# Performance work log

Measured on AMD Instinct MI355X. Metric: run time of the kernel, lower is better.

## Reference

```python
import jax, jax.numpy as jnp
import numpy as np

N, F_IN, HID, HEADS, NEA, E, G = 50000, 32, 64, 2, 2, 800000, 50
SLOPE = 0.2  # leaky_relu negative_slope


def setup_inputs() -> dict:
    key = jax.random.key(0)
    ks = jax.random.split(key, 24)
    x = jax.random.normal(ks[0], (N, F_IN), jnp.float32)
    src = jax.random.randint(ks[1], (E,), 0, N, jnp.int32)
    off = jax.random.randint(ks[2], (E,), 1, N, jnp.int32)
    dst = ((src + off) % N).astype(jnp.int32)  # guaranteed no self loops
    edge_index = jnp.stack([src, dst])
    edge_attr = jax.random.uniform(ks[3], (E, NEA), jnp.float32, 0.5, 3.0)  # distances (reciprocal taken in fwd)
    batch = (jnp.arange(N) // (N // G)).astype(jnp.int32)
    interface_pos = jnp.arange(0, N, 5, dtype=jnp.int32)  # 200 interface nodes/graph

    def glorot(k, shape, fan_in, fan_out):
        s = jnp.sqrt(6.0 / (fan_in + fan_out))
        return jax.random.uniform(k, shape, jnp.float32, -s, s)

    HC = HEADS * HID
    W0 = glorot(ks[4], (F_IN, HC), F_IN, HC)
    attl0 = glorot(ks[5], (HEADS, HID), HID, HID)
    attr0 = glorot(ks[6], (HEADS, HID), HID, HID)
    W12 = glorot(ks[7], (2, HID, HC), HID, HC)
    attl12 = glorot(ks[8], (2, HEADS, HID), HID, HID)
    attr12 = glorot(ks[9], (2, HEADS, HID), HID, HID)
    eW = glorot(ks[10], (3, NEA, HC), NEA, HC)
    eb = jnp.zeros((3, HC), jnp.float32)
    bconv = jnp.zeros((3, HID), jnp.float32)
    gate_w = glorot(ks[11], (HID, 1), HID, 1)
    gate_b = jnp.zeros((1,), jnp.float32)
    lin1_w = glorot(ks[12], (4 * HID, 2 * HID), 4 * HID, 2 * HID)
    lin1_b = jnp.zeros((2 * HID,), jnp.float32)
    lin2_w = glorot(ks[13], (2 * HID, 1), 2 * HID, 1)
    lin2_b = jnp.zeros((1,), jnp.float32)
    return dict(x=x, edge_index=edge_index, edge_attr=edge_attr, batch=batch,
                interface_pos=interface_pos, graph_num=G,
                W0=W0, attl0=attl0, attr0=attr0, W12=W12, attl12=attl12, attr12=attr12,
                eW=eW, eb=eb, bconv=bconv, gate_w=gate_w, gate_b=gate_b,
                lin1_w=lin1_w, lin1_b=lin1_b, lin2_w=lin2_w, lin2_b=lin2_b)


def segment_softmax(e, seg, n):
    m = jax.ops.segment_max(e, seg, num_segments=n)
    ex = jnp.exp(e - m[seg])
    d = jax.ops.segment_sum(ex, seg, num_segments=n)
    return ex / (d[seg] + 1e-16)


def gate_conv(h, W, att_l, att_r, eW, eb, b, src, dst, ea):
    # GATEConv, concat=False, dropout in eval mode (identity)
    n = h.shape[0]
    H, C = att_l.shape
    xl = (h @ W).reshape(n, H, C)                      # lin_l == lin_r
    al = (xl * att_l).sum(-1)                          # [N,H]
    ar = (xl * att_r).sum(-1)
    e = jax.nn.leaky_relu(al[src] + ar[dst], SLOPE)    # [E+N,H]
    alpha = segment_softmax(e, dst, n)
    ee = (ea @ eW + eb).reshape(-1, H, C)              # edge embeddings
    msg = (xl[src] + ee) * alpha[..., None]
    out = jax.ops.segment_sum(msg, dst, num_segments=n)
    return out.mean(1) + b                             # mean over heads + bias


def reference(x, edge_index, edge_attr, batch, interface_pos, graph_num,
              W0, attl0, attr0, W12, attl12, attr12, eW, eb, bconv,
              gate_w, gate_b, lin1_w, lin1_b, lin2_w, lin2_b):
    n = x.shape[0]
    ar_n = jnp.arange(n, dtype=edge_index.dtype)
    src = jnp.concatenate([edge_index[0], ar_n])       # add self loops
    dst = jnp.concatenate([edge_index[1], ar_n])
    ea = jnp.concatenate([1.0 / edge_attr,
                          jnp.zeros((n, edge_attr.shape[1]), edge_attr.dtype)], 0)

    h = jnp.tanh(gate_conv(x, W0, attl0, attr0, eW[0], eb[0], bconv[0], src, dst, ea))
    xmax = h
    for l in range(2):  # num_layers - 1 structurally distinct weight slices
        h = jnp.tanh(gate_conv(h, W12[l], attl12[l], attr12[l],
                               eW[l + 1], eb[l + 1], bconv[l + 1], src, dst, ea))
        xmax = jnp.maximum(xmax, h)                    # JumpingKnowledge('max')

    xi = xmax[interface_pos]                           # [Ni, hidden]
    bi = batch[interface_pos]
    add = jax.ops.segment_sum(xi, bi, num_segments=graph_num)
    cnt = jax.ops.segment_sum(jnp.ones((xi.shape[0],), xi.dtype), bi, num_segments=graph_num)
    mean = add / jnp.maximum(cnt, 1.0)[:, None]
    gate = (xi @ gate_w + gate_b)[:, 0]                # global self-attention gate
    a = segment_softmax(gate, bi, graph_num)
    attp = jax.ops.segment_sum(a[:, None] * xi, bi, num_segments=graph_num)
    mx = jax.ops.segment_max(xi, bi, num_segments=graph_num)
    pooled = jnp.concatenate([add, mean, attp, mx], -1)  # [G, 4*hidden]
    z = jnp.tanh(pooled @ lin1_w + lin1_b)             # dropout eval = identity
    return z @ lin2_w + lin2_b                         # [G, 1]
```

## Files before the change

kernel.cpp:

```cpp
#include <hip/hip_runtime.h>
#include <hip/hip_bf16.h>
#include <hip/hip_fp16.h>
#include <math.h>

#define N_NODES 50000
#define FIN     32
#define HID     64
#define HC      128
#define NE      800000
#define NET     850000
#define NI      10000
#define NG      50
#define PB      8

__device__ __forceinline__ float lrelu(float x) { return x > 0.f ? x : 0.2f * x; }

__device__ __forceinline__ unsigned fenc(float f) {
  unsigned u = __float_as_uint(f);
  return (u & 0x80000000u) ? ~u : (u | 0x80000000u);
}
__device__ __forceinline__ float fdec(unsigned u) {
  return (u & 0x80000000u) ? __uint_as_float(u ^ 0x80000000u) : __uint_as_float(~u);
}

__device__ __forceinline__ float rlf(float v, int l) {
  return __int_as_float(__builtin_amdgcn_readlane(__float_as_int(v), l));
}
__device__ __forceinline__ int rli(int v, int l) {
  return __builtin_amdgcn_readlane(v, l);
}

__global__ void k_histrank(const int* __restrict__ ei, int* __restrict__ deg,
                           int* __restrict__ rank) {
  int e = blockIdx.x * blockDim.x + threadIdx.x;
  if (e >= NET) return;
  int d = (e < NE) ? ei[NE + e] : (e - NE);
  rank[e] = atomicAdd(&deg[d], 1);
}

__global__ void k_base(const int* __restrict__ deg, int* __restrict__ start,
                       int* __restrict__ gcur) {
  __shared__ int buf[256];
  __shared__ int basesh;
  int t = threadIdx.x;
  int i = blockIdx.x * 256 + t;
  int v = (i < N_NODES) ? deg[i] : 0;
  buf[t] = v; __syncthreads();
  for (int off = 1; off < 256; off <<= 1) {
    int a = (t >= off) ? buf[t - off] : 0;
    __syncthreads();
    buf[t] += a;
    __syncthreads();
  }
  if (t == 255) basesh = atomicAdd(gcur, buf[255]);
  __syncthreads();
  if (i < N_NODES) start[i] = basesh + buf[t] - v;
}

__global__ void k_scatter(const int* __restrict__ ei, const float* __restrict__ eattr,
                          const int* __restrict__ start, const int* __restrict__ rank,
                          int2* __restrict__ erec) {
  int e = blockIdx.x * blockDim.x + threadIdx.x;
  if (e >= NET) return;
  int s, d; float ex, ey;
  if (e < NE) {
    s = ei[e]; d = ei[NE + e];
    float2 ea = ((const float2*)eattr)[e];
    ex = 1.0f / ea.x; ey = 1.0f / ea.y;
  } else {
    s = d = e - NE; ex = 0.f; ey = 0.f;
  }
  int pos = start[d] + rank[e];
  __half2 ea2 = __floats2half2_rn(ex, ey);
  erec[pos] = make_int2(s, *(int*)&ea2);
}

template <int F>
__global__ void k_linear(const float* __restrict__ h, const float* __restrict__ W,
                         const float* __restrict__ attl, const float* __restrict__ attr,
                         __half2* __restrict__ xl2h, float* __restrict__ al,
                         float* __restrict__ ar) {
  __shared__ float lds[4][HC];
  const int c = threadIdx.x;
  const int head = c >> 6;
  const int cc = c & 63;
  float wcol[F];
#pragma unroll
  for (int k = 0; k < F; k++) wcol[k] = W[k * HC + c];
  const float attlv = attl[c];
  const float attrv = attr[c];
  for (int g = blockIdx.x; g < N_NODES / 4; g += gridDim.x) {
    const int n0 = g * 4;
    float acc[4] = {0.f, 0.f, 0.f, 0.f};
#pragma unroll
    for (int k4 = 0; k4 < F / 4; k4++) {
      float4 h4[4];
#pragma unroll
      for (int j = 0; j < 4; j++)
        h4[j] = *(const float4*)&h[(n0 + j) * F + k4 * 4];
#pragma unroll
      for (int j = 0; j < 4; j++) {
        acc[j] += h4[j].x * wcol[k4 * 4 + 0];
        acc[j] += h4[j].y * wcol[k4 * 4 + 1];
        acc[j] += h4[j].z * wcol[k4 * 4 + 2];
        acc[j] += h4[j].w * wcol[k4 * 4 + 3];
      }
    }
#pragma unroll
    for (int j = 0; j < 4; j++) {
      float lv = acc[j] * attlv, rv = acc[j] * attrv;
#pragma unroll
      for (int off = 32; off; off >>= 1) {
        lv += __shfl_xor(lv, off, 64);
        rv += __shfl_xor(rv, off, 64);
      }
      if (cc == 0) {
        al[(n0 + j) * 2 + head] = lv;
        ar[(n0 + j) * 2 + head] = rv;
      }
    }
    __syncthreads();
#pragma unroll
    for (int j = 0; j < 4; j++) lds[j][c] = acc[j];
    __syncthreads();
#pragma unroll
    for (int r = 0; r < 2; r++) {
      int idx = c + r * 128;
      int j = idx >> 6, ccc = idx & 63;
      xl2h[(size_t)(n0 + j) * HID + ccc] =
          __floats2half2_rn(lds[j][ccc], lds[j][64 + ccc]);
    }
  }
}

__global__ void k_aggregate(const __half2* __restrict__ xl2h, const float2* __restrict__ al2,
                            const float2* __restrict__ ar2, const int* __restrict__ start,
                            const int* __restrict__ degarr, const int2* __restrict__ erec,
                            const float* __restrict__ eW2, const float* __restrict__ eb1,
                            const float* __restrict__ bconv1, float* __restrict__ hout) {
  const int gid = blockIdx.x * 4 + (threadIdx.x >> 6);
  if (gid >= N_NODES) return;
  const int lane = threadIdx.x & 63;
  const int o0 = start[gid];
  const int deg = degarr[gid];
  const float2 arv = ar2[gid];

  float accA0 = 0.f, accA1 = 0.f, accB0 = 0.f, accB1 = 0.f;
  float ld0 = 0.f, ld1 = 0.f, lex0 = 0.f, ley0 = 0.f, lex1 = 0.f, ley1 = 0.f;
  for (int base = 0; base < deg; base += 64) {
    int j = base + lane;
    int s = 0; float p0 = 0.f, p1 = 0.f;
    if (j < deg) {
      int2 r = erec[o0 + j];
      s = r.x;
      float2 eaf = __half22float2(*(__half2*)&r.y);
      float2 alv = al2[s];
      p0 = __expf(lrelu(alv.x + arv.x));
      p1 = __expf(lrelu(alv.y + arv.y));
      ld0 += p0; ld1 += p1;
      lex0 += p0 * eaf.x; ley0 += p0 * eaf.y;
      lex1 += p1 * eaf.x; ley1 += p1 * eaf.y;
    }
    int slen = min(64, deg - base);
    int j2 = 0;
    for (; j2 + 8 <= slen; j2 += 8) {
      float2 x0 = __half22float2(xl2h[(size_t)rli(s, j2)     * HID + lane]);
      float2 x1 = __half22float2(xl2h[(size_t)rli(s, j2 + 1) * HID + lane]);
      float2 x2 = __half22float2(xl2h[(size_t)rli(s, j2 + 2) * HID + lane]);
      float2 x3 = __half22float2(xl2h[(size_t)rli(s, j2 + 3) * HID + lane]);
      float2 x4 = __half22float2(xl2h[(size_t)rli(s, j2 + 4) * HID + lane]);
      float2 x5 = __half22float2(xl2h[(size_t)rli(s, j2 + 5) * HID + lane]);
      float2 x6 = __half22float2(xl2h[(size_t)rli(s, j2 + 6) * HID + lane]);
      float2 x7 = __half22float2(xl2h[(size_t)rli(s, j2 + 7) * HID + lane]);
      accA0 += rlf(p0, j2)     * x0.x; accA1 += rlf(p1, j2)     * x0.y;
      accB0 += rlf(p0, j2 + 1) * x1.x; accB1 += rlf(p1, j2 + 1) * x1.y;
      accA0 += rlf(p0, j2 + 2) * x2.x; accA1 += rlf(p1, j2 + 2) * x2.y;
      accB0 += rlf(p0, j2 + 3) * x3.x; accB1 += rlf(p1, j2 + 3) * x3.y;
      accA0 += rlf(p0, j2 + 4) * x4.x; accA1 += rlf(p1, j2 + 4) * x4.y;
      accB0 += rlf(p0, j2 + 5) * x5.x; accB1 += rlf(p1, j2 + 5) * x5.y;
      accA0 += rlf(p0, j2 + 6) * x6.x; accA1 += rlf(p1, j2 + 6) * x6.y;
      accB0 += rlf(p0, j2 + 7) * x7.x; accB1 += rlf(p1, j2 + 7) * x7.y;
    }
    for (; j2 + 4 <= slen; j2 += 4) {
      float2 x0 = __half22float2(xl2h[(size_t)rli(s, j2)     * HID + lane]);
      float2 x1 = __half22float2(xl2h[(size_t)rli(s, j2 + 1) * HID + lane]);
      float2 x2 = __half22float2(xl2h[(size_t)rli(s, j2 + 2) * HID + lane]);
      float2 x3 = __half22float2(xl2h[(size_t)rli(s, j2 + 3) * HID + lane]);
      accA0 += rlf(p0, j2)     * x0.x; accA1 += rlf(p1, j2)     * x0.y;
      accB0 += rlf(p0, j2 + 1) * x1.x; accB1 += rlf(p1, j2 + 1) * x1.y;
      accA0 += rlf(p0, j2 + 2) * x2.x; accA1 += rlf(p1, j2 + 2) * x2.y;
      accB0 += rlf(p0, j2 + 3) * x3.x; accB1 += rlf(p1, j2 + 3) * x3.y;
    }
    for (; j2 < slen; j2++) {
      float2 x0 = __half22float2(xl2h[(size_t)rli(s, j2) * HID + lane]);
      accA0 += rlf(p0, j2) * x0.x; accA1 += rlf(p1, j2) * x0.y;
    }
  }
  float acc0 = accA0 + accB0, acc1 = accA1 + accB1;
#pragma unroll
  for (int off = 32; off; off >>= 1) {
    ld0  += __shfl_xor(ld0, off, 64);
    ld1  += __shfl_xor(ld1, off, 64);
    lex0 += __shfl_xor(lex0, off, 64);
    ley0 += __shfl_xor(ley0, off, 64);
    lex1 += __shfl_xor(lex1, off, 64);
    ley1 += __shfl_xor(ley1, off, 64);
  }
  float t0 = acc0 + eW2[lane]      * lex0 + eW2[HC + lane]      * ley0 + eb1[lane]      * ld0;
  float t1 = acc1 + eW2[64 + lane] * lex1 + eW2[HC + 64 + lane] * ley1 + eb1[64 + lane] * ld1;
  float r = 0.5f * (t0 / (ld0 + 1e-16f) + t1 / (ld1 + 1e-16f)) + bconv1[lane];
  hout[(size_t)gid * HID + lane] = tanhf(r);
}

__global__ void k_ranges(const int* __restrict__ ipos, const int* __restrict__ batch,
                         int* __restrict__ gstart) {
  int i = blockIdx.x * blockDim.x + threadIdx.x;
  if (i >= NI) return;
  int bi = batch[ipos[i]];
  int prev = (i > 0) ? batch[ipos[i - 1]] : -1;
  for (int g = prev + 1; g <= bi; g++) gstart[g] = i;
  if (i == NI - 1)
    for (int g = bi + 1; g <= NG; g++) gstart[g] = NI;
}

__global__ void k_pool(const float* __restrict__ h0, const float* __restrict__ h1,
                       const float* __restrict__ h2, const int* __restrict__ ipos,
                       const int* __restrict__ gstart, const float* __restrict__ gate_w,
                       const float* __restrict__ gate_b, float* __restrict__ add,
                       unsigned* __restrict__ mxE, float* __restrict__ cnt,
                       float* __restrict__ attp, float* __restrict__ aden) {
  __shared__ float red[4][3 * HID + 2];
  const int g = blockIdx.x / PB, m = blockIdx.x % PB;
  const int w = threadIdx.x >> 6, lane = threadIdx.x & 63;
  const int s0 = gstart[g], s1 = gstart[g + 1];
  const int len = s1 - s0;
  const int b0 = s0 + (len * m) / PB;
  const int b1 = s0 + (len * (m + 1)) / PB;
  const float gwv = gate_w[lane];
  const float gbv = gate_b[0];

  float padd = 0.f, pmax = -1e30f, pattp = 0.f, paden = 0.f, pcnt = 0.f;
  for (int i = b0 + w; i < b1; i += 4) {
    size_t node = (size_t)ipos[i] * HID + lane;
    float v = fmaxf(fmaxf(h0[node], h1[node]), h2[node]);
    padd += v;
    pmax = fmaxf(pmax, v);
    float gv = v * gwv;
#pragma unroll
    for (int off = 32; off; off >>= 1) gv += __shfl_xor(gv, off, 64);
    float e = __expf(gv + gbv);
    pattp += e * v;
    paden += e;
    pcnt += 1.f;
  }
  red[w][lane] = padd;
  red[w][HID + lane] = pmax;
  red[w][2 * HID + lane] = pattp;
  if (lane == 0) { red[w][3 * HID] = paden; red[w][3 * HID + 1] = pcnt; }
  __syncthreads();
  if (w == 0) {
    float addv  = red[0][lane] + red[1][lane] + red[2][lane] + red[3][lane];
    float maxv  = fmaxf(fmaxf(red[0][HID + lane], red[1][HID + lane]),
                        fmaxf(red[2][HID + lane], red[3][HID + lane]));
    float attpv = red[0][2 * HID + lane] + red[1][2 * HID + lane] +
                  red[2][2 * HID + lane] + red[3][2 * HID + lane];
    atomicAdd(&add[g * HID + lane], addv);
    atomicMax(&mxE[g * HID + lane], fenc(maxv));
    atomicAdd(&attp[g * HID + lane], attpv);
    if (lane == 0) {
      atomicAdd(&aden[g], red[0][3 * HID] + red[1][3 * HID] + red[2][3 * HID] + red[3][3 * HID]);
      atomicAdd(&cnt[g],  red[0][3 * HID + 1] + red[1][3 * HID + 1] +
                          red[2][3 * HID + 1] + red[3][3 * HID + 1]);
    }
  }
}

__global__ void k_final(const float* __restrict__ add, const float* __restrict__ cnt,
                        const float* __restrict__ attp, const float* __restrict__ aden,
                        const unsigned* __restrict__ mxE, const float* __restrict__ lin1_w,
                        const float* __restrict__ lin1_b, const float* __restrict__ lin2_w,
                        const float* __restrict__ lin2_b, float* __restrict__ out) {
  __shared__ float pooled[4 * HID];
  __shared__ float zred[2 * HID];
  int g = blockIdx.x, t = threadIdx.x;
  if (t < HID)            pooled[t] = add[g * HID + t];
  else if (t < 2 * HID)   pooled[t] = add[g * HID + (t - HID)] / fmaxf(cnt[g], 1.f);
  else if (t < 3 * HID)   pooled[t] = attp[g * HID + (t - 2 * HID)] / (aden[g] + 1e-16f);
  else                    pooled[t] = fdec(mxE[g * HID + (t - 3 * HID)]);
  __syncthreads();
  if (t < 2 * HID) {
    float z = lin1_b[t];
    for (int k = 0; k < 4 * HID; k++) z += pooled[k] * lin1_w[k * (2 * HID) + t];
    z = tanhf(z);
    zred[t] = z * lin2_w[t];
  }
  __syncthreads();
  if (t == 0) {
    float s = 0.f;
    for (int k = 0; k < 2 * HID; k++) s += zred[k];
    out[g] = s + lin2_b[0];
  }
}

extern "C" void kernel_launch(void* const* d_in, const int* in_sizes, int n_in,
                              void* d_out, int out_size, void* d_ws, size_t ws_size,
                              hipStream_t stream) {
  const float* x      = (const float*)d_in[0];
  const int*   ei     = (const int*)d_in[1];
  const float* eattr  = (const float*)d_in[2];
  const int*   batch  = (const int*)d_in[3];
  const int*   ipos   = (const int*)d_in[4];
  const float* W0     = (const float*)d_in[6];
  const float* attl0  = (const float*)d_in[7];
  const float* attr0  = (const float*)d_in[8];
  const float* W12    = (const float*)d_in[9];
  const float* attl12 = (const float*)d_in[10];
  const float* attr12 = (const float*)d_in[11];
  const float* eW     = (const float*)d_in[12];
  const float* eb     = (const float*)d_in[13];
  const float* bconv  = (const float*)d_in[14];
  const float* gate_w = (const float*)d_in[15];
  const float* gate_b = (const float*)d_in[16];
  const float* lin1_w = (const float*)d_in[17];
  const float* lin1_b = (const float*)d_in[18];
  const float* lin2_w = (const float*)d_in[19];
  const float* lin2_b = (const float*)d_in[20];
  float* out = (float*)d_out;

  char* ws = (char*)d_ws;
  size_t off = 0;
  auto alloc = [&](size_t elems) {
    void* p = ws + off;
    off += ((elems * 4 + 15) / 16) * 16;
    return p;
  };
  int*      deg    = (int*)alloc(N_NODES);
  int*      gcur   = (int*)alloc(4);
  float*    addp   = (float*)alloc(NG * HID);
  float*    attp   = (float*)alloc(NG * HID);
  unsigned* mxE    = (unsigned*)alloc(NG * HID);
  float*    cnt    = (float*)alloc(64);
  float*    aden   = (float*)alloc(64);
  size_t zbytes = off;
  int*     gstart = (int*)alloc(NG + 4);
  int*     start  = (int*)alloc(N_NODES);
  int*     rank   = (int*)alloc(NET);
  int2*    erec   = (int2*)alloc((size_t)NET * 2);
  __half2* xl2h   = (__half2*)alloc((size_t)N_NODES * HID);
  float*   al     = (float*)alloc((size_t)N_NODES * 2);
  float*   arr    = (float*)alloc((size_t)N_NODES * 2);
  float*   h0     = (float*)alloc((size_t)N_NODES * HID);
  float*   h1     = (float*)alloc((size_t)N_NODES * HID);
  float*   h2     = (float*)alloc((size_t)N_NODES * HID);
  (void)ws_size; (void)in_sizes; (void)n_in; (void)out_size;

  hipMemsetAsync(d_ws, 0, zbytes, stream);
  k_histrank<<<(NET + 255) / 256, 256, 0, stream>>>(ei, deg, rank);
  k_base<<<(N_NODES + 255) / 256, 256, 0, stream>>>(deg, start, gcur);
  k_scatter<<<(NET + 255) / 256, 256, 0, stream>>>(ei, eattr, start, rank, erec);
  k_ranges<<<(NI + 255) / 256, 256, 0, stream>>>(ipos, batch, gstart);

  k_linear<FIN><<<2500, 128, 0, stream>>>(x, W0, attl0, attr0, xl2h, al, arr);
  k_aggregate<<<N_NODES / 4, 256, 0, stream>>>(xl2h, (const float2*)al, (const float2*)arr,
                                               start, deg, erec, eW, eb, bconv, h0);
  k_linear<HID><<<2500, 128, 0, stream>>>(h0, W12, attl12, attr12, xl2h, al, arr);
  k_aggregate<<<N_NODES / 4, 256, 0, stream>>>(xl2h, (const float2*)al, (const float2*)arr,
                                               start, deg, erec, eW + 2 * HC, eb + HC,
                                               bconv + HID, h1);
  k_linear<HID><<<2500, 128, 0, stream>>>(h1, W12 + (size_t)HID * HC,
                                          attl12 + HC, attr12 + HC, xl2h, al, arr);
  k_aggregate<<<N_NODES / 4, 256, 0, stream>>>(xl2h, (const float2*)al, (const float2*)arr,
                                               start, deg, erec, eW + 4 * HC, eb + 2 * HC,
                                               bconv + 2 * HID, h2);

  k_pool<<<NG * PB, 256, 0, stream>>>(h0, h1, h2, ipos, gstart, gate_w, gate_b,
                                      addp, mxE, cnt, attp, aden);
  k_final<<<NG, 256, 0, stream>>>(addp, cnt, attp, aden, mxE, lin1_w, lin1_b, lin2_w, lin2_b, out);
}
```

Baseline: 393.5 us.

## Use MFMA fp16 for node linear and pre-scaled byte offsets in aggregation

New measurement: 341.6 us. -13.2%, faster.

```diff
diff --git a/kernel.cpp b/kernel.cpp
--- a/kernel.cpp
+++ b/kernel.cpp
@@ -13,7 +13,10 @@
 #define NG      50
 #define PB      8
 
-__device__ __forceinline__ float lrelu(float x) { return x > 0.f ? x : 0.2f * x; }
+typedef _Float16 half8 __attribute__((ext_vector_type(8)));
+typedef float float4v __attribute__((ext_vector_type(4)));
+
+__device__ __forceinline__ float lrelu(float x) { return fmaxf(x, 0.2f * x); }
 
 __device__ __forceinline__ unsigned fenc(float f) {
   unsigned u = __float_as_uint(f);
@@ -72,68 +75,88 @@
   }
   int pos = start[d] + rank[e];
   __half2 ea2 = __floats2half2_rn(ex, ey);
-  erec[pos] = make_int2(s, *(int*)&ea2);
+  erec[pos] = make_int2(s << 8, *(int*)&ea2);
 }
 
 template <int F>
-__global__ void k_linear(const float* __restrict__ h, const float* __restrict__ W,
-                         const float* __restrict__ attl, const float* __restrict__ attr,
-                         __half2* __restrict__ xl2h, float* __restrict__ al,
-                         float* __restrict__ ar) {
-  __shared__ float lds[4][HC];
-  const int c = threadIdx.x;
-  const int head = c >> 6;
-  const int cc = c & 63;
-  float wcol[F];
-#pragma unroll
-  for (int k = 0; k < F; k++) wcol[k] = W[k * HC + c];
-  const float attlv = attl[c];
-  const float attrv = attr[c];
-  for (int g = blockIdx.x; g < N_NODES / 4; g += gridDim.x) {
-    const int n0 = g * 4;
-    float acc[4] = {0.f, 0.f, 0.f, 0.f};
-#pragma unroll
-    for (int k4 = 0; k4 < F / 4; k4++) {
-      float4 h4[4];
-#pragma unroll
-      for (int j = 0; j < 4; j++)
-        h4[j] = *(const float4*)&h[(n0 + j) * F + k4 * 4];
-#pragma unroll
-      for (int j = 0; j < 4; j++) {
-        acc[j] += h4[j].x * wcol[k4 * 4 + 0];
-        acc[j] += h4[j].y * wcol[k4 * 4 + 1];
-        acc[j] += h4[j].z * wcol[k4 * 4 + 2];
-        acc[j] += h4[j].w * wcol[k4 * 4 + 3];
-      }
-    }
-#pragma unroll
-    for (int j = 0; j < 4; j++) {
-      float lv = acc[j] * attlv, rv = acc[j] * attrv;
-#pragma unroll
-      for (int off = 32; off; off >>= 1) {
-        lv += __shfl_xor(lv, off, 64);
-        rv += __shfl_xor(rv, off, 64);
-      }
-      if (cc == 0) {
-        al[(n0 + j) * 2 + head] = lv;
-        ar[(n0 + j) * 2 + head] = rv;
-      }
-    }
-    __syncthreads();
-#pragma unroll
-    for (int j = 0; j < 4; j++) lds[j][c] = acc[j];
-    __syncthreads();
-#pragma unroll
-    for (int r = 0; r < 2; r++) {
-      int idx = c + r * 128;
-      int j = idx >> 6, ccc = idx & 63;
-      xl2h[(size_t)(n0 + j) * HID + ccc] =
-          __floats2half2_rn(lds[j][ccc], lds[j][64 + ccc]);
-    }
-  }
-}
-
-__global__ void k_aggregate(const __half2* __restrict__ xl2h, const float2* __restrict__ al2,
+__global__ __launch_bounds__(256) void k_linear_mfma(
+    const float* __restrict__ h, const float* __restrict__ W,
+    const float* __restrict__ attl, const float* __restrict__ attr,
+    __half2* __restrict__ xl2h, float* __restrict__ al, float* __restrict__ ar) {
+  __shared__ _Float16 hA[16 * F];
+  __shared__ _Float16 hC[16 * 128];
+  __shared__ float redl[16 * 4], redr[16 * 4];
+  const int w = threadIdx.x >> 6, lane = threadIdx.x & 63;
+  const int m = lane & 15, q = lane >> 4;
+  const int n0 = blockIdx.x * 16;
+
+  for (int i = threadIdx.x; i < 16 * F; i += 256)
+    hA[i] = (_Float16)h[(size_t)n0 * F + i];
+  __syncthreads();
+
+  half8 a0, a1;
+#pragma unroll
+  for (int j = 0; j < 8; j++) a0[j] = hA[m * F + q * 8 + j];
+  if constexpr (F == 64) {
+#pragma unroll
+    for (int j = 0; j < 8; j++) a1[j] = hA[m * F + 32 + q * 8 + j];
+  }
+
+  const int c0 = w * 32;
+  float4v acc[2];
+  float pl[4] = {0.f, 0.f, 0.f, 0.f}, pr[4] = {0.f, 0.f, 0.f, 0.f};
+#pragma unroll
+  for (int t = 0; t < 2; t++) {
+    const int colg = c0 + t * 16 + m;
+    half8 b0;
+#pragma unroll
+    for (int j = 0; j < 8; j++) b0[j] = (_Float16)W[(q * 8 + j) * HC + colg];
+    float4v z = {0.f, 0.f, 0.f, 0.f};
+    acc[t] = __builtin_amdgcn_mfma_f32_16x16x32_f16(a0, b0, z, 0, 0, 0);
+    if constexpr (F == 64) {
+      half8 b1;
+#pragma unroll
+      for (int j = 0; j < 8; j++) b1[j] = (_Float16)W[(32 + q * 8 + j) * HC + colg];
+      acc[t] = __builtin_amdgcn_mfma_f32_16x16x32_f16(a1, b1, acc[t], 0, 0, 0);
+    }
+    const float atl = attl[colg], atr = attr[colg];
+#pragma unroll
+    for (int reg = 0; reg < 4; reg++) {
+      float val = acc[t][reg];
+      hC[(q * 4 + reg) * 128 + colg] = (_Float16)val;
+      pl[reg] += val * atl;
+      pr[reg] += val * atr;
+    }
+  }
+#pragma unroll
+  for (int off = 1; off < 16; off <<= 1) {
+#pragma unroll
+    for (int reg = 0; reg < 4; reg++) {
+      pl[reg] += __shfl_xor(pl[reg], off, 64);
+      pr[reg] += __shfl_xor(pr[reg], off, 64);
+    }
+  }
+  if (m == 0) {
+#pragma unroll
+    for (int reg = 0; reg < 4; reg++) {
+      redl[(q * 4 + reg) * 4 + w] = pl[reg];
+      redr[(q * 4 + reg) * 4 + w] = pr[reg];
+    }
+  }
+  __syncthreads();
+  if (threadIdx.x < 32) {
+    int node = threadIdx.x >> 1, head = threadIdx.x & 1;
+    al[(n0 + node) * 2 + head] = redl[node * 4 + head * 2] + redl[node * 4 + head * 2 + 1];
+    ar[(n0 + node) * 2 + head] = redr[node * 4 + head * 2] + redr[node * 4 + head * 2 + 1];
+  }
+  for (int i = threadIdx.x; i < 16 * 64; i += 256) {
+    int node = i >> 6, cc = i & 63;
+    xl2h[(size_t)(n0 + node) * HID + cc] =
+        __halves2half2(hC[node * 128 + cc], hC[node * 128 + 64 + cc]);
+  }
+}
+
+__global__ void k_aggregate(const __half2* __restrict__ xl2h, const float* __restrict__ alp,
                             const float2* __restrict__ ar2, const int* __restrict__ start,
                             const int* __restrict__ degarr, const int2* __restrict__ erec,
                             const float* __restrict__ eW2, const float* __restrict__ eb1,
@@ -141,20 +164,23 @@
   const int gid = blockIdx.x * 4 + (threadIdx.x >> 6);
   if (gid >= N_NODES) return;
   const int lane = threadIdx.x & 63;
+  const int lane4 = lane << 2;
   const int o0 = start[gid];
   const int deg = degarr[gid];
   const float2 arv = ar2[gid];
+  const char* xbase = (const char*)xl2h;
+  const char* albase = (const char*)alp;
 
   float accA0 = 0.f, accA1 = 0.f, accB0 = 0.f, accB1 = 0.f;
   float ld0 = 0.f, ld1 = 0.f, lex0 = 0.f, ley0 = 0.f, lex1 = 0.f, ley1 = 0.f;
   for (int base = 0; base < deg; base += 64) {
     int j = base + lane;
-    int s = 0; float p0 = 0.f, p1 = 0.f;
+    int soff = 0; float p0 = 0.f, p1 = 0.f;
     if (j < deg) {
       int2 r = erec[o0 + j];
-      s = r.x;
+      soff = r.x;
       float2 eaf = __half22float2(*(__half2*)&r.y);
-      float2 alv = al2[s];
+      float2 alv = *(const float2*)(albase + (soff >> 5));
       p0 = __expf(lrelu(alv.x + arv.x));
       p1 = __expf(lrelu(alv.y + arv.y));
       ld0 += p0; ld1 += p1;
@@ -164,14 +190,14 @@
     int slen = min(64, deg - base);
     int j2 = 0;
     for (; j2 + 8 <= slen; j2 += 8) {
-      float2 x0 = __half22float2(xl2h[(size_t)rli(s, j2)     * HID + lane]);
-      float2 x1 = __half22float2(xl2h[(size_t)rli(s, j2 + 1) * HID + lane]);
-      float2 x2 = __half22float2(xl2h[(size_t)rli(s, j2 + 2) * HID + lane]);
-      float2 x3 = __half22float2(xl2h[(size_t)rli(s, j2 + 3) * HID + lane]);
-      float2 x4 = __half22float2(xl2h[(size_t)rli(s, j2 + 4) * HID + lane]);
-      float2 x5 = __half22float2(xl2h[(size_t)rli(s, j2 + 5) * HID + lane]);
-      float2 x6 = __half22float2(xl2h[(size_t)rli(s, j2 + 6) * HID + lane]);
-      float2 x7 = __half22float2(xl2h[(size_t)rli(s, j2 + 7) * HID + lane]);
+      float2 x0 = __half22float2(*(const __half2*)(xbase + rli(soff, j2)     + lane4));
+      float2 x1 = __half22float2(*(const __half2*)(xbase + rli(soff, j2 + 1) + lane4));
+      float2 x2 = __half22float2(*(const __half2*)(xbase + rli(soff, j2 + 2) + lane4));
+      float2 x3 = __half22float2(*(const __half2*)(xbase + rli(soff, j2 + 3) + lane4));
+      float2 x4 = __half22float2(*(const __half2*)(xbase + rli(soff, j2 + 4) + lane4));
+      float2 x5 = __half22float2(*(const __half2*)(xbase + rli(soff, j2 + 5) + lane4));
+      float2 x6 = __half22float2(*(const __half2*)(xbase + rli(soff, j2 + 6) + lane4));
+      float2 x7 = __half22float2(*(const __half2*)(xbase + rli(soff, j2 + 7) + lane4));
       accA0 += rlf(p0, j2)     * x0.x; accA1 += rlf(p1, j2)     * x0.y;
       accB0 += rlf(p0, j2 + 1) * x1.x; accB1 += rlf(p1, j2 + 1) * x1.y;
       accA0 += rlf(p0, j2 + 2) * x2.x; accA1 += rlf(p1, j2 + 2) * x2.y;
@@ -182,17 +208,17 @@
       accB0 += rlf(p0, j2 + 7) * x7.x; accB1 += rlf(p1, j2 + 7) * x7.y;
     }
     for (; j2 + 4 <= slen; j2 += 4) {
-      float2 x0 = __half22float2(xl2h[(size_t)rli(s, j2)     * HID + lane]);
-      float2 x1 = __half22float2(xl2h[(size_t)rli(s, j2 + 1) * HID + lane]);
-      float2 x2 = __half22float2(xl2h[(size_t)rli(s, j2 + 2) * HID + lane]);
-      float2 x3 = __half22float2(xl2h[(size_t)rli(s, j2 + 3) * HID + lane]);
+      float2 x0 = __half22float2(*(const __half2*)(xbase + rli(soff, j2)     + lane4));
+      float2 x1 = __half22float2(*(const __half2*)(xbase + rli(soff, j2 + 1) + lane4));
+      float2 x2 = __half22float2(*(const __half2*)(xbase + rli(soff, j2 + 2) + lane4));
+      float2 x3 = __half22float2(*(const __half2*)(xbase + rli(soff, j2 + 3) + lane4));
       accA0 += rlf(p0, j2)     * x0.x; accA1 += rlf(p1, j2)     * x0.y;
       accB0 += rlf(p0, j2 + 1) * x1.x; accB1 += rlf(p1, j2 + 1) * x1.y;
       accA0 += rlf(p0, j2 + 2) * x2.x; accA1 += rlf(p1, j2 + 2) * x2.y;
       accB0 += rlf(p0, j2 + 3) * x3.x; accB1 += rlf(p1, j2 + 3) * x3.y;
     }
     for (; j2 < slen; j2++) {
-      float2 x0 = __half22float2(xl2h[(size_t)rli(s, j2) * HID + lane]);
+      float2 x0 = __half22float2(*(const __half2*)(xbase + rli(soff, j2) + lane4));
       accA0 += rlf(p0, j2) * x0.x; accA1 += rlf(p1, j2) * x0.y;
     }
   }
@@ -360,16 +386,16 @@
   k_scatter<<<(NET + 255) / 256, 256, 0, stream>>>(ei, eattr, start, rank, erec);
   k_ranges<<<(NI + 255) / 256, 256, 0, stream>>>(ipos, batch, gstart);
 
-  k_linear<FIN><<<2500, 128, 0, stream>>>(x, W0, attl0, attr0, xl2h, al, arr);
-  k_aggregate<<<N_NODES / 4, 256, 0, stream>>>(xl2h, (const float2*)al, (const float2*)arr,
+  k_linear_mfma<FIN><<<N_NODES / 16, 256, 0, stream>>>(x, W0, attl0, attr0, xl2h, al, arr);
+  k_aggregate<<<N_NODES / 4, 256, 0, stream>>>(xl2h, al, (const float2*)arr,
                                                start, deg, erec, eW, eb, bconv, h0);
-  k_linear<HID><<<2500, 128, 0, stream>>>(h0, W12, attl12, attr12, xl2h, al, arr);
-  k_aggregate<<<N_NODES / 4, 256, 0, stream>>>(xl2h, (const float2*)al, (const float2*)arr,
+  k_linear_mfma<HID><<<N_NODES / 16, 256, 0, stream>>>(h0, W12, attl12, attr12, xl2h, al, arr);
+  k_aggregate<<<N_NODES / 4, 256, 0, stream>>>(xl2h, al, (const float2*)arr,
                                                start, deg, erec, eW + 2 * HC, eb + HC,
                                                bconv + HID, h1);
-  k_linear<HID><<<2500, 128, 0, stream>>>(h1, W12 + (size_t)HID * HC,
-                                          attl12 + HC, attr12 + HC, xl2h, al, arr);
-  k_aggregate<<<N_NODES / 4, 256, 0, stream>>>(xl2h, (const float2*)al, (const float2*)arr,
+  k_linear_mfma<HID><<<N_NODES / 16, 256, 0, stream>>>(h1, W12 + (size_t)HID * HC,
+                                                       attl12 + HC, attr12 + HC, xl2h, al, arr);
+  k_aggregate<<<N_NODES / 4, 256, 0, stream>>>(xl2h, al, (const float2*)arr,
                                                start, deg, erec, eW + 4 * HC, eb + 2 * HC,
                                                bconv + 2 * HID, h2);
 
```
